# Kernel tuning notes

Hardware: AMD Instinct MI355X
Metric: run time of the kernel (lower is better)

The kernel has to match this reference:

```python
import jax, jax.numpy as jnp
import numpy as np

N_NODES = 50000
N_EDGES = 160000
D = 512
N_GRAPHS = 64
EPS = 1e-5


def setup_inputs() -> dict:
    key = jax.random.key(0)
    ks = jax.random.split(key, 8)
    node = jax.random.normal(ks[0], (N_NODES, D), dtype=jnp.float32)
    edge_index = jax.random.randint(ks[1], (2, N_EDGES), 0, N_NODES, dtype=jnp.int64)
    edge_attr = jax.random.uniform(ks[2], (N_EDGES,), dtype=jnp.float32)
    batch_ptr = jnp.sort(jax.random.randint(ks[3], (N_NODES,), 0, N_GRAPHS, dtype=jnp.int64))
    W = jax.random.normal(ks[4], (D, D), dtype=jnp.float32) / np.float32(np.sqrt(D))
    b = jnp.zeros((D,), dtype=jnp.float32)
    gn_weight = jnp.ones((D,), dtype=jnp.float32)
    gn_bias = jnp.zeros((D,), dtype=jnp.float32)
    gn_mean_scale = jnp.ones((D,), dtype=jnp.float32)
    return {"node": node, "edge_attr": edge_attr, "W": W, "b": b,
            "gn_weight": gn_weight, "gn_bias": gn_bias, "gn_mean_scale": gn_mean_scale,
            "edge_index": edge_index, "batch_ptr": batch_ptr}


def _gcn_conv(x, edge_index, edge_weight, W, b):
    # x: [N, D]. PyG GCNConv(normalize=True): lin -> add self-loops -> D^-1/2 A D^-1/2 -> + bias
    x = x @ W  # [N, D]
    loop = jnp.arange(N_NODES, dtype=edge_index.dtype)
    row = jnp.concatenate([edge_index[0], loop])  # source
    col = jnp.concatenate([edge_index[1], loop])  # target
    w = jnp.concatenate([edge_weight, jnp.ones((N_NODES,), dtype=x.dtype)])
    deg = jax.ops.segment_sum(w, col, num_segments=N_NODES)  # weighted in-degree incl. self-loop
    dis = jnp.where(deg > 0, jax.lax.rsqrt(deg), 0.0)
    norm = dis[row] * w * dis[col]  # [E+N]
    msgs = x[row] * norm[:, None]  # gather + scale
    out = jax.ops.segment_sum(msgs, col, num_segments=N_NODES)  # scatter-add
    return out + b


def _graph_norm(x, batch, weight, bias, mean_scale):
    # PyG GraphNorm: per-graph mean/var over nodes, learnable mean scale alpha
    ones = jnp.ones((x.shape[0],), dtype=x.dtype)
    count = jax.ops.segment_sum(ones, batch, num_segments=N_GRAPHS)  # [G]
    count = jnp.maximum(count, 1.0)[:, None]
    mean = jax.ops.segment_sum(x, batch, num_segments=N_GRAPHS) / count  # [G, D]
    centered = x - mean[batch] * mean_scale  # [N, D]
    var = jax.ops.segment_sum(centered * centered, batch, num_segments=N_GRAPHS) / count
    inv_std = jax.lax.rsqrt(var + EPS)  # [G, D]
    return weight * centered * inv_std[batch] + bias


def reference(node, edge_attr, W, b, gn_weight, gn_bias, gn_mean_scale, edge_index, batch_ptr):
    conv = _gcn_conv(node, edge_index, edge_attr, W, b)
    h = node + conv  # skip_connection=True
    h = _graph_norm(h, batch_ptr, gn_weight, gn_bias, gn_mean_scale)
    return jax.nn.relu(h)
```

## Files before the change

### kernel.cpp

```cpp
#include <hip/hip_runtime.h>


#define N_NODES 50000
#define PADN    50048
#define N_EDGES 160000
#define DIM 512
#define N_GRAPHS 64
#define EPSV 1e-5f
#define NBLK 196

typedef short short8 __attribute__((ext_vector_type(8)));
typedef float floatx4 __attribute__((ext_vector_type(4)));

__device__ __forceinline__ unsigned short f2bf(float x) {
    unsigned int u = __float_as_uint(x);
    u += 0x7FFFu + ((u >> 16) & 1u);
    return (unsigned short)(u >> 16);
}
__device__ __forceinline__ float bf2f(unsigned short s) {
    return __uint_as_float(((unsigned int)s) << 16);
}

__global__ __launch_bounds__(256) void k_init(float* __restrict__ deg,
                                              float* __restrict__ Sx,
                                              float* __restrict__ Sxx,
                                              float* __restrict__ cntg,
                                              int* __restrict__ ecnt) {
    int i = blockIdx.x * 256 + threadIdx.x;
    if (i < N_NODES) { deg[i] = 1.0f; ecnt[i] = 0; }
    if (i < N_GRAPHS * DIM) { Sx[i] = 0.f; Sxx[i] = 0.f; }
    if (i < N_GRAPHS) cntg[i] = 0.f;
}

__global__ __launch_bounds__(256) void k_deg(const int* __restrict__ ei,
                                             const float* __restrict__ ew,
                                             float* __restrict__ deg,
                                             int* __restrict__ ecnt) {
    int e = blockIdx.x * 256 + threadIdx.x;
    if (e < N_EDGES) {
        int c = ei[N_EDGES + e];
        atomicAdd(&deg[c], ew[e]);
        atomicAdd(&ecnt[c], 1);
    }
}

__global__ __launch_bounds__(256) void k_scanA(const int* __restrict__ ecnt,
                                               int* __restrict__ bsum) {
    int i = blockIdx.x * 256 + threadIdx.x;
    int v = (i < N_NODES) ? ecnt[i] : 0;
#pragma unroll
    for (int off = 32; off; off >>= 1) v += __shfl_down(v, off, 64);
    __shared__ int ws[4];
    if ((threadIdx.x & 63) == 0) ws[threadIdx.x >> 6] = v;
    __syncthreads();
    if (threadIdx.x == 0) bsum[blockIdx.x] = ws[0] + ws[1] + ws[2] + ws[3];
}

__global__ __launch_bounds__(256) void k_scanB(const int* __restrict__ bsum,
                                               int* __restrict__ bbase) {
    __shared__ int s[256];
    int t = threadIdx.x;
    int v = (t < NBLK) ? bsum[t] : 0;
    s[t] = v;
    __syncthreads();
#pragma unroll
    for (int off = 1; off < 256; off <<= 1) {
        int u = (t >= off) ? s[t - off] : 0;
        __syncthreads();
        s[t] += u;
        __syncthreads();
    }
    if (t <= NBLK) bbase[t] = (t == 0) ? 0 : s[t - 1];
}

__global__ __launch_bounds__(256) void k_scanC(const int* __restrict__ ecnt,
                                               const int* __restrict__ bbase,
                                               int* __restrict__ rowptr,
                                               int* __restrict__ cursor,
                                               float* __restrict__ deg) {
    __shared__ int s[256];
    int t = threadIdx.x;
    int i = blockIdx.x * 256 + t;
    int v = (i < N_NODES) ? ecnt[i] : 0;
    s[t] = v;
    __syncthreads();
#pragma unroll
    for (int off = 1; off < 256; off <<= 1) {
        int u = (t >= off) ? s[t - off] : 0;
        __syncthreads();
        s[t] += u;
        __syncthreads();
    }
    int excl = s[t] - v + bbase[blockIdx.x];
    if (i <= N_NODES) rowptr[i] = excl;
    if (i < N_NODES) {
        cursor[i] = excl;
        deg[i] = rsqrtf(deg[i]);
    }
}

__global__ __launch_bounds__(256) void k_fill(const int* __restrict__ ei,
                                              const float* __restrict__ ew,
                                              const float* __restrict__ dis,
                                              int* __restrict__ cursor,
                                              int* __restrict__ srcs,
                                              float* __restrict__ wts) {
    int e = blockIdx.x * 256 + threadIdx.x;
    if (e >= N_EDGES) return;
    int r = ei[e];
    int c = ei[N_EDGES + e];
    int pos = atomicAdd(&cursor[c], 1);
    srcs[pos] = r;
    wts[pos] = ew[e] * dis[r];
}

__global__ __launch_bounds__(256) void k_cast(const float* __restrict__ node,
                                              short* __restrict__ nodeB) {
    size_t idx = (size_t)blockIdx.x * 256 + threadIdx.x;
    size_t base = idx * 8;
    int row = (int)(base >> 9);
    int4 o;
    if (row >= N_NODES) {
        o = make_int4(0, 0, 0, 0);
    } else {
        float4 a = *(const float4*)&node[base];
        float4 c = *(const float4*)&node[base + 4];
        o.x = ((unsigned)f2bf(a.y) << 16) | f2bf(a.x);
        o.y = ((unsigned)f2bf(a.w) << 16) | f2bf(a.z);
        o.z = ((unsigned)f2bf(c.y) << 16) | f2bf(c.x);
        o.w = ((unsigned)f2bf(c.w) << 16) | f2bf(c.z);
    }
    *(int4*)&nodeB[base] = o;
}

__global__ __launch_bounds__(256) void k_prep_w(const float* __restrict__ W,
                                                short* __restrict__ Wt) {
    int i = blockIdx.x * 256 + threadIdx.x;
    int k = i >> 9, n = i & 511;
    Wt[n * 512 + k] = (short)f2bf(W[i]);
}

__global__ __launch_bounds__(256) void k_gemm_mfma(const short* __restrict__ Abf,
                                                   const short* __restrict__ Bt,
                                                   short* __restrict__ Cbf) {
    __shared__ short As[128 * 64];
    __shared__ short Bs[128 * 64];
    const int tid  = threadIdx.x;
    const int wave = tid >> 6;
    const int lane = tid & 63;
    const int l16  = lane & 15;
    const int quad = lane >> 4;
    const int row0 = blockIdx.y * 128;
    const int col0 = blockIdx.x * 128;
    const int mb = (wave >> 1) * 64;
    const int nb = (wave & 1) * 64;

    floatx4 acc[4][4];
    const floatx4 z = {0.f, 0.f, 0.f, 0.f};
#pragma unroll
    for (int i = 0; i < 4; ++i)
#pragma unroll
        for (int j = 0; j < 4; ++j) acc[i][j] = z;

    const int srow = lane >> 3;
    const int scol = (lane & 7) * 8;

    for (int kk = 0; kk < DIM; kk += 64) {
#pragma unroll
        for (int j = 0; j < 4; ++j) {
            int seg = wave * 4 + j;
            int r = seg * 8 + srow;
            __builtin_amdgcn_global_load_lds(
                (const __attribute__((address_space(1))) void*)(Abf + (size_t)(row0 + r) * DIM + kk + scol),
                (__attribute__((address_space(3))) void*)(As + seg * 512 + lane * 8),
                16, 0, 0);
            __builtin_amdgcn_global_load_lds(
                (const __attribute__((address_space(1))) void*)(Bt + (size_t)(col0 + r) * DIM + kk + scol),
                (__attribute__((address_space(3))) void*)(Bs + seg * 512 + lane * 8),
                16, 0, 0);
        }
        __syncthreads();
#pragma unroll
        for (int kh = 0; kh < 2; ++kh) {
            short8 af[4], bfr[4];
#pragma unroll
            for (int i = 0; i < 4; ++i)
                af[i] = *(const short8*)&As[(mb + i * 16 + l16) * 64 + kh * 32 + quad * 8];
#pragma unroll
            for (int j = 0; j < 4; ++j)
                bfr[j] = *(const short8*)&Bs[(nb + j * 16 + l16) * 64 + kh * 32 + quad * 8];
#pragma unroll
            for (int i = 0; i < 4; ++i)
#pragma unroll
                for (int j = 0; j < 4; ++j)
                    acc[i][j] = __builtin_amdgcn_mfma_f32_16x16x32_bf16(af[i], bfr[j], acc[i][j], 0, 0, 0);
        }
        __syncthreads();
    }
#pragma unroll
    for (int i = 0; i < 4; ++i)
#pragma unroll
        for (int j = 0; j < 4; ++j) {
            int col = col0 + nb + j * 16 + l16;
#pragma unroll
            for (int r = 0; r < 4; ++r) {
                int row = row0 + mb + i * 16 + quad * 4 + r;
                Cbf[(size_t)row * DIM + col] = (short)f2bf(acc[i][j][r]);
            }
        }
}

__global__ __launch_bounds__(256) void k_gather(const int* __restrict__ rowptr,
                                                const int* __restrict__ srcs,
                                                const float* __restrict__ wts,
                                                const short* __restrict__ xWb,
                                                const float* __restrict__ node,
                                                const float* __restrict__ b,
                                                const float* __restrict__ dis,
                                                float* __restrict__ out) {
    int n = blockIdx.x * 2 + (threadIdx.x >> 7);
    int q = (threadIdx.x & 127) * 4;
    if (n >= N_NODES) return;
    float dn = dis[n];
    int lo = rowptr[n], hi = rowptr[n + 1];
    ushort4 xs = *(const ushort4*)&xWb[(size_t)n * DIM + q];
    float4 acc;
    acc.x = dn * bf2f(xs.x); acc.y = dn * bf2f(xs.y);
    acc.z = dn * bf2f(xs.z); acc.w = dn * bf2f(xs.w);
    for (int i = lo; i < hi; ++i) {
        int s = srcs[i];
        float w = wts[i];
        ushort4 v = *(const ushort4*)&xWb[(size_t)s * DIM + q];
        acc.x += w * bf2f(v.x); acc.y += w * bf2f(v.y);
        acc.z += w * bf2f(v.z); acc.w += w * bf2f(v.w);
    }
    float4 nd = *(const float4*)&node[(size_t)n * DIM + q];
    float4 bb = *(const float4*)&b[q];
    float4 r;
    r.x = nd.x + bb.x + dn * acc.x;
    r.y = nd.y + bb.y + dn * acc.y;
    r.z = nd.z + bb.z + dn * acc.z;
    r.w = nd.w + bb.w + dn * acc.w;
    *(float4*)&out[(size_t)n * DIM + q] = r;
}

__global__ __launch_bounds__(256) void k_stats(const float* __restrict__ h,
                                               const int* __restrict__ batch,
                                               float* __restrict__ Sx,
                                               float* __restrict__ Sxx,
                                               float* __restrict__ cntg) {
    const int CH = 32;
    int n0 = blockIdx.x * CH;
    if (n0 >= N_NODES) return;
    int nEnd = n0 + CH; if (nEnd > N_NODES) nEnd = N_NODES;
    int t = threadIdx.x;
    float sx0 = 0.f, sx1 = 0.f, sxx0 = 0.f, sxx1 = 0.f;
    int cur = batch[n0];
    int seg = 0;
    for (int n = n0; n < nEnd; ++n) {
        int g = batch[n];
        if (g != cur) {
            atomicAdd(&Sx[cur * DIM + t], sx0);
            atomicAdd(&Sx[cur * DIM + t + 256], sx1);
            atomicAdd(&Sxx[cur * DIM + t], sxx0);
            atomicAdd(&Sxx[cur * DIM + t + 256], sxx1);
            if (t == 0) atomicAdd(&cntg[cur], (float)seg);
            sx0 = sx1 = sxx0 = sxx1 = 0.f; seg = 0; cur = g;
        }
        float a = h[(size_t)n * DIM + t];
        float c2 = h[(size_t)n * DIM + t + 256];
        sx0 += a;  sxx0 += a * a;
        sx1 += c2; sxx1 += c2 * c2;
        seg++;
    }
    atomicAdd(&Sx[cur * DIM + t], sx0);
    atomicAdd(&Sx[cur * DIM + t + 256], sx1);
    atomicAdd(&Sxx[cur * DIM + t], sxx0);
    atomicAdd(&Sxx[cur * DIM + t + 256], sxx1);
    if (t == 0) atomicAdd(&cntg[cur], (float)seg);
}

__global__ __launch_bounds__(256) void k_fin(const float* __restrict__ Sx,
                                             const float* __restrict__ Sxx,
                                             const float* __restrict__ cntg,
                                             const float* __restrict__ alpha,
                                             float* __restrict__ mA,
                                             float* __restrict__ inv) {
    int i = blockIdx.x * 256 + threadIdx.x;
    if (i >= N_GRAPHS * DIM) return;
    int d = i & (DIM - 1);
    int g = i >> 9;
    float c = fmaxf(cntg[g], 1.0f);
    float m = Sx[i] / c;
    float ma = m * alpha[d];
    float var = Sxx[i] / c - 2.f * m * ma + ma * ma;
    mA[i] = ma;
    inv[i] = rsqrtf(var + EPSV);
}

__global__ __launch_bounds__(256) void k_norm(float* __restrict__ out,
                                              const int* __restrict__ batch,
                                              const float* __restrict__ mA,
                                              const float* __restrict__ inv,
                                              const float* __restrict__ gw,
                                              const float* __restrict__ gb) {
    size_t idx = (size_t)blockIdx.x * 256 + threadIdx.x;
    int n = (int)(idx >> 7);
    int q = ((int)idx & 127) * 4;
    if (n >= N_NODES) return;
    int g = batch[n];
    float4 h = *(const float4*)&out[(size_t)n * DIM + q];
    float4 ma = *(const float4*)&mA[(size_t)g * DIM + q];
    float4 iv = *(const float4*)&inv[(size_t)g * DIM + q];
    float4 w4 = *(const float4*)&gw[q];
    float4 b4 = *(const float4*)&gb[q];
    float4 r;
    r.x = fmaxf(0.f, (h.x - ma.x) * iv.x * w4.x + b4.x);
    r.y = fmaxf(0.f, (h.y - ma.y) * iv.y * w4.y + b4.y);
    r.z = fmaxf(0.f, (h.z - ma.z) * iv.z * w4.z + b4.z);
    r.w = fmaxf(0.f, (h.w - ma.w) * iv.w * w4.w + b4.w);
    *(float4*)&out[(size_t)n * DIM + q] = r;
}

extern "C" void kernel_launch(void* const* d_in, const int* in_sizes, int n_in,
                              void* d_out, int out_size, void* d_ws, size_t ws_size,
                              hipStream_t stream) {
    const float* node  = (const float*)d_in[0];
    const float* eattr = (const float*)d_in[1];
    const float* W     = (const float*)d_in[2];
    const float* b     = (const float*)d_in[3];
    const float* gw    = (const float*)d_in[4];
    const float* gb    = (const float*)d_in[5];
    const float* alpha = (const float*)d_in[6];
    const int*   ei    = (const int*)d_in[7];
    const int*   batch = (const int*)d_in[8];
    float* out = (float*)d_out;

    short* nodeB = (short*)d_ws;
    short* xWb   = nodeB + (size_t)PADN * DIM;
    short* Wt    = xWb + (size_t)PADN * DIM;
    float* dis   = (float*)(Wt + DIM * DIM);
    float* Sx    = dis + N_NODES;
    float* Sxx   = Sx + N_GRAPHS * DIM;
    float* cntg  = Sxx + N_GRAPHS * DIM;
    float* mA    = cntg + 64;
    float* inv   = mA + N_GRAPHS * DIM;
    float* wts   = inv + N_GRAPHS * DIM;
    int* ecnt    = (int*)(wts + N_EDGES);
    int* rowptr  = ecnt + N_NODES;
    int* cursor  = rowptr + N_NODES + 1;
    int* srcs    = cursor + N_NODES;
    int* bsum    = srcs + N_EDGES;
    int* bbase   = bsum + NBLK;

    k_init<<<196, 256, 0, stream>>>(dis, Sx, Sxx, cntg, ecnt);
    k_deg<<<(N_EDGES + 255) / 256, 256, 0, stream>>>(ei, eattr, dis, ecnt);
    k_scanA<<<NBLK, 256, 0, stream>>>(ecnt, bsum);
    k_scanB<<<1, 256, 0, stream>>>(bsum, bbase);
    k_scanC<<<NBLK, 256, 0, stream>>>(ecnt, bbase, rowptr, cursor, dis);
    k_fill<<<(N_EDGES + 255) / 256, 256, 0, stream>>>(ei, eattr, dis, cursor, srcs, wts);
    k_cast<<<(PADN * DIM / 8 + 255) / 256, 256, 0, stream>>>(node, nodeB);
    k_prep_w<<<(DIM * DIM + 255) / 256, 256, 0, stream>>>(W, Wt);
    dim3 ggrid(4, PADN / 128);
    k_gemm_mfma<<<ggrid, 256, 0, stream>>>(nodeB, Wt, xWb);
    k_gather<<<N_NODES / 2, 256, 0, stream>>>(rowptr, srcs, wts, xWb, node, b, dis, out);
    k_stats<<<(N_NODES + 31) / 32, 256, 0, stream>>>(out, batch, Sx, Sxx, cntg);
    k_fin<<<128, 256, 0, stream>>>(Sx, Sxx, cntg, alpha, mA, inv);
    k_norm<<<25000, 256, 0, stream>>>(out, batch, mA, inv, gw, gb);
}
```

Baseline: 418.8 us.

## Fuse gather with GraphNorm statistics and store intermediate h in bf16

```diff
diff --git a/kernel.cpp b/kernel.cpp
--- a/kernel.cpp
+++ b/kernel.cpp
@@ -210,74 +210,84 @@
         }
 }
 
-__global__ __launch_bounds__(256) void k_gather(const int* __restrict__ rowptr,
-                                                const int* __restrict__ srcs,
-                                                const float* __restrict__ wts,
-                                                const short* __restrict__ xWb,
-                                                const float* __restrict__ node,
-                                                const float* __restrict__ b,
-                                                const float* __restrict__ dis,
-                                                float* __restrict__ out) {
-    int n = blockIdx.x * 2 + (threadIdx.x >> 7);
-    int q = (threadIdx.x & 127) * 4;
-    if (n >= N_NODES) return;
-    float dn = dis[n];
-    int lo = rowptr[n], hi = rowptr[n + 1];
-    ushort4 xs = *(const ushort4*)&xWb[(size_t)n * DIM + q];
-    float4 acc;
-    acc.x = dn * bf2f(xs.x); acc.y = dn * bf2f(xs.y);
-    acc.z = dn * bf2f(xs.z); acc.w = dn * bf2f(xs.w);
-    for (int i = lo; i < hi; ++i) {
-        int s = srcs[i];
-        float w = wts[i];
-        ushort4 v = *(const ushort4*)&xWb[(size_t)s * DIM + q];
-        acc.x += w * bf2f(v.x); acc.y += w * bf2f(v.y);
-        acc.z += w * bf2f(v.z); acc.w += w * bf2f(v.w);
-    }
-    float4 nd = *(const float4*)&node[(size_t)n * DIM + q];
+__global__ __launch_bounds__(256) void k_gather_stats(
+        const int* __restrict__ rowptr,
+        const int* __restrict__ srcs,
+        const float* __restrict__ wts,
+        const short* __restrict__ xWb,
+        short* __restrict__ nodeB,
+        const float* __restrict__ b,
+        const float* __restrict__ dis,
+        const int* __restrict__ batch,
+        float* __restrict__ Sx,
+        float* __restrict__ Sxx,
+        float* __restrict__ cntg) {
+    const int half = threadIdx.x >> 7;
+    const int q = (threadIdx.x & 127) * 4;
+    const int lead = (threadIdx.x & 127) == 0;
+    const int n0 = blockIdx.x * 32;
     float4 bb = *(const float4*)&b[q];
-    float4 r;
-    r.x = nd.x + bb.x + dn * acc.x;
-    r.y = nd.y + bb.y + dn * acc.y;
-    r.z = nd.z + bb.z + dn * acc.z;
-    r.w = nd.w + bb.w + dn * acc.w;
-    *(float4*)&out[(size_t)n * DIM + q] = r;
-}
-
-__global__ __launch_bounds__(256) void k_stats(const float* __restrict__ h,
-                                               const int* __restrict__ batch,
-                                               float* __restrict__ Sx,
-                                               float* __restrict__ Sxx,
-                                               float* __restrict__ cntg) {
-    const int CH = 32;
-    int n0 = blockIdx.x * CH;
-    if (n0 >= N_NODES) return;
-    int nEnd = n0 + CH; if (nEnd > N_NODES) nEnd = N_NODES;
-    int t = threadIdx.x;
-    float sx0 = 0.f, sx1 = 0.f, sxx0 = 0.f, sxx1 = 0.f;
-    int cur = batch[n0];
-    int seg = 0;
-    for (int n = n0; n < nEnd; ++n) {
+    float sx0 = 0.f, sx1 = 0.f, sx2 = 0.f, sx3 = 0.f;
+    float xx0 = 0.f, xx1 = 0.f, xx2 = 0.f, xx3 = 0.f;
+    int cur = -1, cnt = 0;
+    for (int r = 0; r < 16; ++r) {
+        int n = n0 + r * 2 + half;
+        if (n >= N_NODES) break;
         int g = batch[n];
         if (g != cur) {
-            atomicAdd(&Sx[cur * DIM + t], sx0);
-            atomicAdd(&Sx[cur * DIM + t + 256], sx1);
-            atomicAdd(&Sxx[cur * DIM + t], sxx0);
-            atomicAdd(&Sxx[cur * DIM + t + 256], sxx1);
-            if (t == 0) atomicAdd(&cntg[cur], (float)seg);
-            sx0 = sx1 = sxx0 = sxx1 = 0.f; seg = 0; cur = g;
-        }
-        float a = h[(size_t)n * DIM + t];
-        float c2 = h[(size_t)n * DIM + t + 256];
-        sx0 += a;  sxx0 += a * a;
-        sx1 += c2; sxx1 += c2 * c2;
-        seg++;
-    }
-    atomicAdd(&Sx[cur * DIM + t], sx0);
-    atomicAdd(&Sx[cur * DIM + t + 256], sx1);
-    atomicAdd(&Sxx[cur * DIM + t], sxx0);
-    atomicAdd(&Sxx[cur * DIM + t + 256], sxx1);
-    if (t == 0) atomicAdd(&cntg[cur], (float)seg);
+            if (cur >= 0) {
+                atomicAdd(&Sx[cur * DIM + q + 0], sx0);
+                atomicAdd(&Sx[cur * DIM + q + 1], sx1);
+                atomicAdd(&Sx[cur * DIM + q + 2], sx2);
+                atomicAdd(&Sx[cur * DIM + q + 3], sx3);
+                atomicAdd(&Sxx[cur * DIM + q + 0], xx0);
+                atomicAdd(&Sxx[cur * DIM + q + 1], xx1);
+                atomicAdd(&Sxx[cur * DIM + q + 2], xx2);
+                atomicAdd(&Sxx[cur * DIM + q + 3], xx3);
+                if (lead) atomicAdd(&cntg[cur], (float)cnt);
+                sx0 = sx1 = sx2 = sx3 = 0.f;
+                xx0 = xx1 = xx2 = xx3 = 0.f;
+                cnt = 0;
+            }
+            cur = g;
+        }
+        float dn = dis[n];
+        int lo = rowptr[n], hi = rowptr[n + 1];
+        ushort4 xs = *(const ushort4*)&xWb[(size_t)n * DIM + q];
+        float a0 = dn * bf2f(xs.x), a1 = dn * bf2f(xs.y);
+        float a2 = dn * bf2f(xs.z), a3 = dn * bf2f(xs.w);
+        for (int i = lo; i < hi; ++i) {
+            int s = srcs[i];
+            float w = wts[i];
+            ushort4 v = *(const ushort4*)&xWb[(size_t)s * DIM + q];
+            a0 += w * bf2f(v.x); a1 += w * bf2f(v.y);
+            a2 += w * bf2f(v.z); a3 += w * bf2f(v.w);
+        }
+        ushort4 nv = *(const ushort4*)&nodeB[(size_t)n * DIM + q];
+        float h0 = bf2f(nv.x) + bb.x + dn * a0;
+        float h1 = bf2f(nv.y) + bb.y + dn * a1;
+        float h2 = bf2f(nv.z) + bb.z + dn * a2;
+        float h3 = bf2f(nv.w) + bb.w + dn * a3;
+        sx0 += h0; xx0 += h0 * h0;
+        sx1 += h1; xx1 += h1 * h1;
+        sx2 += h2; xx2 += h2 * h2;
+        sx3 += h3; xx3 += h3 * h3;
+        cnt++;
+        ushort4 hv;
+        hv.x = f2bf(h0); hv.y = f2bf(h1); hv.z = f2bf(h2); hv.w = f2bf(h3);
+        *(ushort4*)&nodeB[(size_t)n * DIM + q] = hv;
+    }
+    if (cur >= 0) {
+        atomicAdd(&Sx[cur * DIM + q + 0], sx0);
+        atomicAdd(&Sx[cur * DIM + q + 1], sx1);
+        atomicAdd(&Sx[cur * DIM + q + 2], sx2);
+        atomicAdd(&Sx[cur * DIM + q + 3], sx3);
+        atomicAdd(&Sxx[cur * DIM + q + 0], xx0);
+        atomicAdd(&Sxx[cur * DIM + q + 1], xx1);
+        atomicAdd(&Sxx[cur * DIM + q + 2], xx2);
+        atomicAdd(&Sxx[cur * DIM + q + 3], xx3);
+        if (lead) atomicAdd(&cntg[cur], (float)cnt);
+    }
 }
 
 __global__ __launch_bounds__(256) void k_fin(const float* __restrict__ Sx,
@@ -298,27 +308,28 @@
     inv[i] = rsqrtf(var + EPSV);
 }
 
-__global__ __launch_bounds__(256) void k_norm(float* __restrict__ out,
+__global__ __launch_bounds__(256) void k_norm(const short* __restrict__ hB,
                                               const int* __restrict__ batch,
                                               const float* __restrict__ mA,
                                               const float* __restrict__ inv,
                                               const float* __restrict__ gw,
-                                              const float* __restrict__ gb) {
+                                              const float* __restrict__ gb,
+                                              float* __restrict__ out) {
     size_t idx = (size_t)blockIdx.x * 256 + threadIdx.x;
     int n = (int)(idx >> 7);
     int q = ((int)idx & 127) * 4;
     if (n >= N_NODES) return;
     int g = batch[n];
-    float4 h = *(const float4*)&out[(size_t)n * DIM + q];
+    ushort4 hv = *(const ushort4*)&hB[(size_t)n * DIM + q];
     float4 ma = *(const float4*)&mA[(size_t)g * DIM + q];
     float4 iv = *(const float4*)&inv[(size_t)g * DIM + q];
     float4 w4 = *(const float4*)&gw[q];
     float4 b4 = *(const float4*)&gb[q];
     float4 r;
-    r.x = fmaxf(0.f, (h.x - ma.x) * iv.x * w4.x + b4.x);
-    r.y = fmaxf(0.f, (h.y - ma.y) * iv.y * w4.y + b4.y);
-    r.z = fmaxf(0.f, (h.z - ma.z) * iv.z * w4.z + b4.z);
-    r.w = fmaxf(0.f, (h.w - ma.w) * iv.w * w4.w + b4.w);
+    r.x = fmaxf(0.f, (bf2f(hv.x) - ma.x) * iv.x * w4.x + b4.x);
+    r.y = fmaxf(0.f, (bf2f(hv.y) - ma.y) * iv.y * w4.y + b4.y);
+    r.z = fmaxf(0.f, (bf2f(hv.z) - ma.z) * iv.z * w4.z + b4.z);
+    r.w = fmaxf(0.f, (bf2f(hv.w) - ma.w) * iv.w * w4.w + b4.w);
     *(float4*)&out[(size_t)n * DIM + q] = r;
 }
 
@@ -363,8 +374,9 @@
     k_prep_w<<<(DIM * DIM + 255) / 256, 256, 0, stream>>>(W, Wt);
     dim3 ggrid(4, PADN / 128);
     k_gemm_mfma<<<ggrid, 256, 0, stream>>>(nodeB, Wt, xWb);
-    k_gather<<<N_NODES / 2, 256, 0, stream>>>(rowptr, srcs, wts, xWb, node, b, dis, out);
-    k_stats<<<(N_NODES + 31) / 32, 256, 0, stream>>>(out, batch, Sx, Sxx, cntg);
+    k_gather_stats<<<(N_NODES + 31) / 32, 256, 0, stream>>>(rowptr, srcs, wts, xWb,
+                                                            nodeB, b, dis, batch,
+                                                            Sx, Sxx, cntg);
     k_fin<<<128, 256, 0, stream>>>(Sx, Sxx, cntg, alpha, mA, inv);
-    k_norm<<<25000, 256, 0, stream>>>(out, batch, mA, inv, gw, gb);
-}
+    k_norm<<<25000, 256, 0, stream>>>(nodeB, batch, mA, inv, gw, gb, out);
+}
```

After: 416.7 us. Within noise of the previous version (-0.5%).
